# Kernel optimization log

Hardware: AMD Instinct MI355X
Metric: run time of the kernel (lower is better)

The kernel has to match this reference:

```python
import jax, jax.numpy as jnp
import numpy as np

B, C, H, W = 8, 64, 128, 128
NH, OPH = 4, 16
MX, MY = 32, 17  # n_modes=(32,32) -> modes_y = 32//2+1
NPAT_S, NPAT_F = 10000, 5000
ED_S, ED_F = 64, 32


def setup_inputs() -> dict:
    ks = jax.random.split(jax.random.key(0), 16)
    n = lambda k, s, sc=1.0: jax.random.normal(k, s, dtype=jnp.float32) * sc
    z = lambda s: jnp.zeros(s, jnp.float32)
    return dict(
        x=n(ks[0], (B, C, H, W)),
        se_emb=n(ks[1], (NPAT_S, ED_S)),
        se_w=n(ks[2], (ED_S, C), 0.1), se_b=z(C),
        mhf_wr=n(ks[3], (NH, C, OPH, MX, MY), 0.01),
        mhf_wi=n(ks[4], (NH, C, OPH, MX, MY), 0.01),
        mhf_bias=z(C),
        sp_emb=n(ks[5], (NPAT_F, ED_F)),
        sp_wr=n(ks[6], (ED_F, C * MX * MY), 0.05), sp_br=z(C * MX * MY),
        sp_wi=n(ks[7], (ED_F, C * MX * MY), 0.05), sp_bi=z(C * MX * MY),
        gate_w1=n(ks[8], (3 * C, 64), 0.05), gate_b1=z(64),
        gate_w2=n(ks[9], (64, 3), 0.05), gate_b2=z(3),
        skip_w=n(ks[10], (C, C), 0.05), skip_b=z(C),
        norm_g=jnp.ones(C), norm_b=z(C),
        mlp_w1=n(ks[11], (C, 2 * C), 0.05), mlp_b1=z(2 * C),
        mlp_w2=n(ks[12], (2 * C, C), 0.05), mlp_b2=z(C),
    )


def _gelu(v):
    return jax.nn.gelu(v, approximate=False)


def _block(x, se_emb, se_w, se_b, mhf_wr, mhf_wi, mhf_bias, sp_emb, sp_wr, sp_br,
           sp_wi, sp_bi, gate_w1, gate_b1, gate_w2, gate_b2, skip_w, skip_b,
           norm_g, norm_b, mlp_w1, mlp_b1, mlp_w2, mlp_b2):
    Bq, Cq, Hq, Wq = x.shape
    # --- SpatialEngram: quantization is elementwise, so sum over window entries
    # equals 3x3 box-sum of the quantized padded field (identical integers,
    # avoids materializing the (B,C,H,W,3,3) unfold tensor).
    xp = jnp.pad(x, ((0, 0), (0, 0), (1, 1), (1, 1)), mode='edge')
    q = (xp * 100.0).astype(jnp.int32)  # trunc toward zero, same as torch .long()
    hv = jnp.zeros((Bq, Cq, Hq, Wq), jnp.int32)
    for i in range(3):
        for j in range(3):
            hv = hv + q[:, :, i:i + Hq, j:j + Wq]
    idx = (jnp.abs(hv) % NPAT_S).astype(jnp.float32).mean(axis=1).astype(jnp.int32)  # (B,H,W)
    spatial = jnp.moveaxis(se_emb[idx] @ se_w + se_b, -1, 1)  # (B,C,H,W)
    # --- MHF multi-head spectral conv (all heads in one einsum; concat == reshape)
    xf = jnp.fft.rfft2(x, norm='ortho')          # (B,C,H,W//2+1) complex64
    lo = xf[:, :, :MX, :MY]
    wc = (mhf_wr + 1j * mhf_wi).astype(lo.dtype)
    of = jnp.einsum('biXY,hioXY->bhoXY', lo, wc).reshape(Bq, Cq, MX, MY)
    full = jnp.zeros((Bq, Cq, Hq, Wq // 2 + 1), lo.dtype).at[:, :, :MX, :MY].set(of)
    mhf = jnp.fft.irfft2(full, s=(Hq, Wq), norm='ortho') + mhf_bias[:, None, None]
    # --- SpectralEngram: per-sample hash of low-freq magnitude -> embedding -> freq proj
    mag = jnp.abs(lo).mean(axis=(1, 2, 3))                       # (B,)
    fidx = (mag * 1000.0).astype(jnp.int32) % NPAT_F
    fe = sp_emb[fidx]                                            # (B,ED_F)
    re = (fe @ sp_wr + sp_br).reshape(Bq, Cq, MX, MY)
    im = (fe @ sp_wi + sp_bi).reshape(Bq, Cq, MX, MY)
    full2 = jnp.zeros((Bq, Cq, Hq, Wq // 2 + 1), lo.dtype).at[:, :, :MX, :MY].set(re + 1j * im)
    spec = jnp.fft.irfft2(full2, s=(Hq, Wq), norm='ortho')
    # --- gated fusion
    gate_in = jnp.concatenate([spatial.mean((2, 3)), mhf.mean((2, 3)), spec.mean((2, 3))], axis=-1)
    gw = jax.nn.softmax(_gelu(gate_in @ gate_w1 + gate_b1) @ gate_w2 + gate_b2, axis=-1)
    a = gw[:, 0, None, None, None]
    bt = gw[:, 1, None, None, None]
    gm = gw[:, 2, None, None, None]
    fused = a * spatial + bt * mhf + gm * spec
    y = fused + jnp.einsum('bihw,io->bohw', x, skip_w) + skip_b[:, None, None]
    # --- GroupNorm(1,C) + 1x1-conv channel MLP (dropout=0)
    mu = y.mean((1, 2, 3), keepdims=True)
    var = y.var((1, 2, 3), keepdims=True)
    yn = (y - mu) * jax.lax.rsqrt(var + 1e-5) * norm_g[:, None, None] + norm_b[:, None, None]
    h = _gelu(jnp.einsum('bihw,io->bohw', yn, mlp_w1) + mlp_b1[:, None, None])
    h = jnp.einsum('bihw,io->bohw', h, mlp_w2) + mlp_b2[:, None, None]
    return y + h


def reference(x, se_emb, se_w, se_b, mhf_wr, mhf_wi, mhf_bias, sp_emb, sp_wr, sp_br,
              sp_wi, sp_bi, gate_w1, gate_b1, gate_w2, gate_b2, skip_w, skip_b,
              norm_g, norm_b, mlp_w1, mlp_b1, mlp_w2, mlp_b2):
    return _block(x, se_emb, se_w, se_b, mhf_wr, mhf_wi, mhf_bias, sp_emb, sp_wr, sp_br,
                  sp_wi, sp_bi, gate_w1, gate_b1, gate_w2, gate_b2, skip_w, skip_b,
                  norm_g, norm_b, mlp_w1, mlp_b1, mlp_w2, mlp_b2)
```

## Files before the change

### kernel.cpp

```cpp
#include <hip/hip_runtime.h>
#include <hip/hip_bf16.h>
#include <math.h>

#define B_ 8
#define C_ 64
#define H_ 128
#define W_ 128
#define NH_ 4
#define OPH_ 16
#define MX_ 32
#define MY_ 17
#define NPAT_F 5000
#define ED_F 32
#define XY_ (MX_*MY_)
#define HW_ (H_*W_)
#define NE_ (B_*C_*H_*W_)

#define OFF_LO     0u
#define OFF_T2     2228224u
#define OFF_FMHF   11141120u
#define OFF_FSPEC  13369344u
#define OFF_IDX    15597568u

typedef __hip_bfloat16 bf16;

template<typename T>
__device__ __forceinline__ float ldt(const void* p, int i){ return (float)(((const T*)p)[i]); }

__device__ __forceinline__ float gelu_f(float a){
  return 0.5f*a*(1.0f + erff(a*0.70710678118654752f));
}

__global__ void k_det(const void* ng, int* flag, double* dmag){
  if(threadIdx.x==0) *flag = (((const unsigned*)ng)[0] == 0x3F800000u) ? 1 : 0;
  if(threadIdx.x<B_) dmag[threadIdx.x] = 0.0;
}

template<typename T>
__device__ __forceinline__ void hash_body(const void* x, int* idx, int b, int h, int w){
  int hm = h>0 ? h-1 : 0, hp = h<127 ? h+1 : 127;
  int wm = w>0 ? w-1 : 0, wp = w<127 ? w+1 : 127;
  int s = 0;
  for(int c=0;c<C_;++c){
    const int base = ((b*C_+c)*H_)*W_;
    const int r0 = base + hm*W_, r1 = base + h*W_, r2 = base + hp*W_;
    int q = (int)(ldt<T>(x,r0+wm)*100.0f) + (int)(ldt<T>(x,r0+w)*100.0f) + (int)(ldt<T>(x,r0+wp)*100.0f)
          + (int)(ldt<T>(x,r1+wm)*100.0f) + (int)(ldt<T>(x,r1+w)*100.0f) + (int)(ldt<T>(x,r1+wp)*100.0f)
          + (int)(ldt<T>(x,r2+wm)*100.0f) + (int)(ldt<T>(x,r2+w)*100.0f) + (int)(ldt<T>(x,r2+wp)*100.0f);
    s += (q < 0 ? -q : q) % 10000;
  }
  idx[(b*H_+h)*W_+w] = s >> 6;
}
__global__ __launch_bounds__(128) void k_hash(const void* x, int* idx, const int* flg){
  int h = blockIdx.x, b = blockIdx.y, w = threadIdx.x;
  if(*flg) hash_body<float>(x, idx, b, h, w); else hash_body<bf16>(x, idx, b, h, w);
}

__global__ __launch_bounds__(256) void k_f1(const void* __restrict__ x, double* __restrict__ t1,
                                            const int* flg, int b0){
  __shared__ float xs[64*130];
  __shared__ double2 csd[128];
  int t = threadIdx.x;
  if(t<128){ double a = (double)t * (6.283185307179586476925286766559/128.0); csd[t] = make_double2(cos(a), sin(a)); }
  int hhalf = blockIdx.x, bcl = blockIdx.y;
  int h0 = hhalf << 6;
  long xbase = ((long)(b0*C_ + bcl)*H_ + h0)*W_;
  if(*flg){
    const float* xp = (const float*)x + xbase;
    for(int i=t;i<4096;i+=256){
      int r=i>>6, w2=(i&63)<<1;
      *(float2*)(xs + r*130 + w2) = *(const float2*)(xp + r*W_ + w2);
    }
  } else {
    const unsigned short* xp = (const unsigned short*)x + xbase;
    for(int i=t;i<4096;i+=256){
      int r=i>>6, w2=(i&63)<<1;
      unsigned raw = *(const unsigned*)(xp + r*W_ + w2);
      float2 v; v.x = __uint_as_float(raw<<16); v.y = __uint_as_float(raw & 0xffff0000u);
      *(float2*)(xs + r*130 + w2) = v;
    }
  }
  __syncthreads();
  for(int o=t;o<MY_*64;o+=256){
    int ky = o>>6, hr = o&63;
    const float* xr = xs + hr*130;
    double ar=0.0, ai=0.0;
    int m = 0;
    for(int w=0;w<W_;++w){
      double v = (double)xr[w];
      double2 cs2 = csd[m];
      ar = fma(v, cs2.x, ar);
      ai = fma(-v, cs2.y, ai);
      m = (m + ky) & 127;
    }
    int tt = (bcl*MY_ + ky)*H_ + (h0 + hr);
    *(double2*)(t1 + 2*tt) = make_double2(ar, ai);
  }
}

__global__ __launch_bounds__(576) void k_f2(const double* __restrict__ t1, float* __restrict__ lo, int b0){
  __shared__ double2 ts[MY_*129];
  __shared__ double2 csd[128];
  int t = threadIdx.x;
  if(t<128){ double a = (double)t * (6.283185307179586476925286766559/128.0); csd[t] = make_double2(cos(a), sin(a)); }
  int bcl = blockIdx.x;
  const double2* tg = (const double2*)t1 + (size_t)bcl*MY_*H_;
  for(int i=t;i<MY_*H_;i+=576){ int ky=i>>7, hh=i&127; ts[ky*129+hh] = tg[i]; }
  __syncthreads();
  if(t < 544){
    int ky = t % MY_, kx = t / MY_;
    const double2* tr = ts + ky*129;
    double ar=0.0, ai=0.0;
    int m = 0;
    for(int h=0;h<H_;++h){
      double2 v = tr[h];
      double2 cs2 = csd[m];
      double vr = v.x, vi = v.y;
      double cc = cs2.x, ss = cs2.y;
      ar += vr*cc + vi*ss;
      ai += vi*cc - vr*ss;
      m = (m + kx) & 127;
    }
    int g = (b0*C_ + bcl)*XY_ + kx*MY_ + ky;
    *(float2*)(lo + 2*g) = make_float2((float)(ar*(1.0/128.0)), (float)(ai*(1.0/128.0)));
  }
}

template<typename T>
__device__ __forceinline__ void spatial_load_w(const void* se_w, const void* se_b, float wsm[64][64], float* sb, int t){
  for(int i=t;i<4096;i+=256) wsm[i>>6][i&63] = ldt<T>(se_w, i);
  if(t<64) sb[t] = ldt<T>(se_b, t);
}
template<typename T>
__device__ __forceinline__ void spatial_load_emb(const void* se_emb, const int* ibs, float emb[32][65], int w0, int t){
  for(int i=t;i<2048;i+=256){ int wl_=i>>6, e=i&63; emb[wl_][e] = ldt<T>(se_emb, ibs[w0+wl_]*64 + e); }
}
__global__ __launch_bounds__(256) void k_spatial(const void* se_emb, const void* se_w, const void* se_b,
                                                 const int* __restrict__ idx, bf16* __restrict__ spatial,
                                                 const int* flg){
  __shared__ float wsm[64][64];
  __shared__ float emb[32][65];
  __shared__ float sb[64];
  __shared__ int ibs[128];
  int b = blockIdx.x >> 7, h = blockIdx.x & 127, t = threadIdx.x;
  int f = *flg;
  if(f) spatial_load_w<float>(se_w, se_b, wsm, sb, t); else spatial_load_w<bf16>(se_w, se_b, wsm, sb, t);
  if(t<128) ibs[t] = idx[(b*H_+h)*W_ + t];
  __syncthreads();
  for(int chunk=0; chunk<4; ++chunk){
    int w0 = chunk*32;
    if(f) spatial_load_emb<float>(se_emb, ibs, emb, w0, t); else spatial_load_emb<bf16>(se_emb, ibs, emb, w0, t);
    __syncthreads();
    for(int i=t;i<2048;i+=256){
      int cc=i>>5, wl_=i&31;
      float acc = sb[cc];
      #pragma unroll 8
      for(int e=0;e<64;++e) acc = fmaf(emb[wl_][e], wsm[e][cc], acc);
      spatial[((b*C_+cc)*H_+h)*W_ + w0+wl_] = __float2bfloat16(acc);
    }
    __syncthreads();
  }
}

__global__ __launch_bounds__(256) void k_mag(const float* __restrict__ lo, double* __restrict__ dmag){
  int b = blockIdx.y, t = threadIdx.x;
  const float* p = lo + b*C_*XY_*2;
  double s = 0.0;
  for(int i = blockIdx.x*256 + t; i < C_*XY_; i += 17*256){
    double re = p[2*i], im = p[2*i+1];
    s += sqrt(re*re + im*im);
  }
  __shared__ double sh[256];
  sh[t] = s; __syncthreads();
  for(int k=128;k>0;k>>=1){ if(t<k) sh[t]+=sh[t+k]; __syncthreads(); }
  if(t==0) atomicAdd(&dmag[b], sh[0]);
}

template<typename T>
__device__ __forceinline__ void specf_body(const void* sp_emb, const void* sp_wr, const void* sp_br,
                                           const void* sp_wi, const void* sp_bi, const double* dmag,
                                           float* fspec, float* fe, int b, int j, int t){
  double mag = dmag[b] / (double)(C_*XY_);
  int fv = ((int)(mag*1000.0)) % NPAT_F;
  fv = fv < 0 ? 0 : (fv >= NPAT_F ? NPAT_F-1 : fv);
  if(t < ED_F) fe[t] = ldt<T>(sp_emb, fv*ED_F + t);
  __syncthreads();
  float re = ldt<T>(sp_br, j), im = ldt<T>(sp_bi, j);
  #pragma unroll 8
  for(int e=0;e<ED_F;++e){
    float f = fe[e];
    re = fmaf(f, ldt<T>(sp_wr, e*(C_*XY_)+j), re);
    im = fmaf(f, ldt<T>(sp_wi, e*(C_*XY_)+j), im);
  }
  int o = b*C_*XY_ + j;
  fspec[2*o] = re; fspec[2*o+1] = im;
}
__global__ __launch_bounds__(256) void k_specf(const void* sp_emb, const void* sp_wr, const void* sp_br,
                                               const void* sp_wi, const void* sp_bi, const double* __restrict__ dmag,
                                               float* __restrict__ fspec, const int* flg){
  __shared__ float fe[ED_F];
  int b = blockIdx.y;
  int j = blockIdx.x*256 + threadIdx.x;
  if(*flg) specf_body<float>(sp_emb, sp_wr, sp_br, sp_wi, sp_bi, dmag, fspec, fe, b, j, threadIdx.x);
  else     specf_body<bf16 >(sp_emb, sp_wr, sp_br, sp_wi, sp_bi, dmag, fspec, fe, b, j, threadIdx.x);
}

template<typename T>
__device__ __forceinline__ void mhf_body(const float* lp, const void* wr, const void* wi,
                                         float* fmhf, int b, int co){
  int hh = co >> 4, o = co & 15;
  for(int xy = threadIdx.x; xy < XY_; xy += 256){
    float ar=0.f, ai=0.f;
    for(int i=0;i<C_;++i){
      float lr = lp[(i*XY_+xy)*2], li = lp[(i*XY_+xy)*2+1];
      int widx = ((hh*C_ + i)*OPH_ + o)*XY_ + xy;
      float wre = ldt<T>(wr, widx), wim = ldt<T>(wi, widx);
      ar += lr*wre - li*wim;
      ai += lr*wim + li*wre;
    }
    int oo = (b*C_ + co)*XY_ + xy;
    fmhf[2*oo] = ar; fmhf[2*oo+1] = ai;
  }
}
__global__ __launch_bounds__(256) void k_mhf(const float* __restrict__ lo, const void* wr, const void* wi,
                                             float* __restrict__ fmhf, const int* flg){
  int b = blockIdx.y, co = blockIdx.x;
  const float* lp = lo + b*C_*XY_*2;
  if(*flg) mhf_body<float>(lp, wr, wi, fmhf, b, co); else mhf_body<bf16>(lp, wr, wi, fmhf, b, co);
}

__global__ __launch_bounds__(256) void k_gmean(const bf16* __restrict__ spatial, float* __restrict__ smean){
  int cch = blockIdx.x, b = blockIdx.y, t = threadIdx.x;
  const unsigned short* p = (const unsigned short*)(spatial + (size_t)(b*C_+cch)*HW_);
  float s = 0.f;
  for(int i=t;i<HW_/8;i+=256){
    uint4 v = *(const uint4*)(p + (size_t)i*8);
    s += __uint_as_float(v.x<<16) + __uint_as_float(v.x&0xffff0000u)
       + __uint_as_float(v.y<<16) + __uint_as_float(v.y&0xffff0000u)
       + __uint_as_float(v.z<<16) + __uint_as_float(v.z&0xffff0000u)
       + __uint_as_float(v.w<<16) + __uint_as_float(v.w&0xffff0000u);
  }
  __shared__ float sh[256];
  sh[t]=s; __syncthreads();
  for(int k=128;k>0;k>>=1){ if(t<k) sh[t]+=sh[t+k]; __syncthreads(); }
  if(t==0) smean[b*C_+cch] = sh[0]*(1.0f/16384.0f);
}

template<typename T>
__device__ __forceinline__ void gate_body(const float* smean, const float* fmhf, const float* fspec,
                                          const void* mbias, const void* w1, const void* b1,
                                          const void* w2, const void* b2,
                                          float* gw, float* ssum, float* ssq,
                                          float* gin, float* hid, int b, int t){
  gin[t]      = smean[b*C_+t];
  gin[64+t]   = fmhf [(b*C_+t)*XY_*2] * (1.0f/128.0f) + ldt<T>(mbias, t);
  gin[128+t]  = fspec[(b*C_+t)*XY_*2] * (1.0f/128.0f);
  __syncthreads();
  float acc = ldt<T>(b1, t);
  for(int k=0;k<192;++k) acc = fmaf(gin[k], ldt<T>(w1, k*64+t), acc);
  hid[t] = gelu_f(acc);
  __syncthreads();
  if(t==0){
    float o[3];
    for(int j=0;j<3;++j){
      float a = ldt<T>(b2, j);
      for(int k=0;k<64;++k) a += hid[k]*ldt<T>(w2, k*3+j);
      o[j]=a;
    }
    float mx = fmaxf(o[0], fmaxf(o[1], o[2]));
    float e0=expf(o[0]-mx), e1=expf(o[1]-mx), e2=expf(o[2]-mx);
    float sum=e0+e1+e2;
    gw[b*3+0]=e0/sum; gw[b*3+1]=e1/sum; gw[b*3+2]=e2/sum;
    ssum[b]=0.f; ssq[b]=0.f;
  }
}
__global__ __launch_bounds__(64) void k_gate(const float* __restrict__ smean, const float* __restrict__ fmhf,
                                             const float* __restrict__ fspec, const void* mbias,
                                             const void* w1, const void* b1, const void* w2, const void* b2,
                                             float* __restrict__ gw, float* __restrict__ ssum,
                                             float* __restrict__ ssq, const int* flg){
  __shared__ float gin[192];
  __shared__ float hid[64];
  int b = blockIdx.x, t = threadIdx.x;
  if(*flg) gate_body<float>(smean, fmhf, fspec, mbias, w1, b1, w2, b2, gw, ssum, ssq, gin, hid, b, t);
  else     gate_body<bf16 >(smean, fmhf, fspec, mbias, w1, b1, w2, b2, gw, ssum, ssq, gin, hid, b, t);
}

__global__ __launch_bounds__(256) void k_comb(const float* __restrict__ fmhf, const float* __restrict__ fspec,
                                              const float* __restrict__ gw, float* __restrict__ t2){
  __shared__ float Gr[XY_], Gi[XY_], cs[128], sn[128];
  int c = blockIdx.x, b = blockIdx.y, t = threadIdx.x;
  if(t<128) __sincosf((float)t * 0.04908738521234052f, &sn[t], &cs[t]);
  float bt=gw[b*3+1], gm=gw[b*3+2];
  for(int i=t;i<XY_;i+=256){
    int o = ((b*C_+c)*XY_+i)*2;
    Gr[i] = bt*fmhf[o]   + gm*fspec[o];
    Gi[i] = bt*fmhf[o+1] + gm*fspec[o+1];
  }
  __syncthreads();
  for(int i=t;i<MY_*H_;i+=256){
    int hh = i & 127, ky = i >> 7;
    float ar=0.f, ai=0.f;
    for(int kx=0;kx<MX_;++kx){
      int m = (kx*hh)&127;
      float cc=cs[m], ss=sn[m];
      float fr=Gr[kx*MY_+ky], fi=Gi[kx*MY_+ky];
      ar += fr*cc - fi*ss;
      ai += fr*ss + fi*cc;
    }
    int e = (((b*C_+c)*MY_+ky)*H_ + hh)*2;
    t2[e]=ar; t2[e+1]=ai;
  }
}

template<typename T>
__device__ __forceinline__ void fuse_body(const void* x, const void* skw, const void* skb, const void* mbias,
                                          bf16* sp_y, const float* t2, const float* gw,
                                          float* ssum, float* ssq,
                                          float wl[64][64], float Ur[64][17], float Ui[64][17],
                                          float* cs, float* sn, float* sb, float* mb,
                                          float* s1, float* s2, int b, int h, int t){
  int w = t & 127, half = t >> 7;
  if(t<128) __sincosf((float)t * 0.04908738521234052f, &sn[t], &cs[t]);
  for(int i=t;i<4096;i+=256) wl[i>>6][i&63] = ldt<T>(skw, i);
  if(t<64){ sb[t]=ldt<T>(skb,t); mb[t]=ldt<T>(mbias,t); }
  for(int i=t;i<C_*MY_;i+=256){
    int cc=i/MY_, ky=i%MY_;
    int e = (((b*C_+cc)*MY_+ky)*H_ + h)*2;
    Ur[cc][ky]=t2[e]; Ui[cc][ky]=t2[e+1];
  }
  float ga=gw[b*3], gbv=gw[b*3+1];
  __syncthreads();
  int c0 = half*32;
  float acc[32];
  #pragma unroll
  for(int j=0;j<32;++j) acc[j]=sb[c0+j];
  int xb = (b*C_*H_ + h)*W_ + w;
  for(int k=0;k<64;++k){
    float xv = ldt<T>(x, xb + k*HW_);
    #pragma unroll
    for(int j=0;j<32;++j) acc[j] = fmaf(xv, wl[k][c0+j], acc[j]);
  }
  float ls=0.f, lq=0.f;
  for(int j=0;j<32;++j){
    int cc=c0+j;
    float vr = Ur[cc][0];
    #pragma unroll
    for(int ky=1;ky<MY_;++ky){
      int m=(ky*w)&127;
      vr += 2.0f*(Ur[cc][ky]*cs[m] - Ui[cc][ky]*sn[m]);
    }
    int gi = ((b*C_+cc)*H_+h)*W_+w;
    float v = ga*__bfloat162float(sp_y[gi]) + vr*(1.0f/128.0f) + gbv*mb[cc] + acc[j];
    sp_y[gi] = __float2bfloat16(v);
    ls += v; lq = fmaf(v, v, lq);
  }
  s1[t]=ls; s2[t]=lq; __syncthreads();
  for(int k=128;k>0;k>>=1){ if(t<k){ s1[t]+=s1[t+k]; s2[t]+=s2[t+k]; } __syncthreads(); }
  if(t==0){ atomicAdd(&ssum[b], s1[0]); atomicAdd(&ssq[b], s2[0]); }
}
__global__ __launch_bounds__(256) void k_fuse(const void* x, const void* skw, const void* skb, const void* mbias,
                                              bf16* __restrict__ sp_y, const float* __restrict__ t2,
                                              const float* __restrict__ gw,
                                              float* __restrict__ ssum, float* __restrict__ ssq, const int* flg){
  __shared__ float wl[64][64];
  __shared__ float Ur[64][17], Ui[64][17];
  __shared__ float cs[128], sn[128];
  __shared__ float sb[64], mb[64];
  __shared__ float s1[256], s2[256];
  int h = blockIdx.x, b = blockIdx.y, t = threadIdx.x;
  if(*flg) fuse_body<float>(x, skw, skb, mbias, sp_y, t2, gw, ssum, ssq, wl, Ur, Ui, cs, sn, sb, mb, s1, s2, b, h, t);
  else     fuse_body<bf16 >(x, skw, skb, mbias, sp_y, t2, gw, ssum, ssq, wl, Ur, Ui, cs, sn, sb, mb, s1, s2, b, h, t);
}

__global__ void k_stats(const float* __restrict__ ssum, const float* __restrict__ ssq,
                        float* __restrict__ mu, float* __restrict__ rs){
  int b = threadIdx.x;
  if(b < B_){
    float m = ssum[b] * (1.0f/1048576.0f);
    float v = ssq[b] * (1.0f/1048576.0f) - m*m;
    mu[b] = m;
    rs[b] = rsqrtf(v + 1e-5f);
  }
}

template<typename T>
__device__ __forceinline__ void mlp_body(const bf16* __restrict__ y, float mu, float rs,
                                         const void* ng, const void* nb, const void* w1, const void* b1,
                                         const void* w2, const void* b2, float* __restrict__ out,
                                         float* __restrict__ yn_s, float* __restrict__ w_s,
                                         float* __restrict__ h2_s,
                                         int b, int h, int w0, int t){
  const int tx = t & 15, ty = t >> 4;
  const int p0 = ty << 2;
  const int ybase = (b*C_*H_ + h)*W_ + w0;

  for(int i=t;i<8192;i+=256) w_s[i] = ldt<T>(w1, i);
  for(int it=0; it<4; ++it){
    int chunk = t + (it<<8);
    int c = chunk >> 4, p4 = (chunk & 15) << 2;
    const unsigned short* yp = (const unsigned short*)y + ybase + c*HW_ + p4;
    uint2 raw = *(const uint2*)yp;
    float g = ldt<T>(ng, c), nbv = ldt<T>(nb, c);
    float sc = rs*g;
    float4 o;
    o.x = (__uint_as_float(raw.x<<16)          - mu)*sc + nbv;
    o.y = (__uint_as_float(raw.x & 0xffff0000u)- mu)*sc + nbv;
    o.z = (__uint_as_float(raw.y<<16)          - mu)*sc + nbv;
    o.w = (__uint_as_float(raw.y & 0xffff0000u)- mu)*sc + nbv;
    *(float4*)(yn_s + c*68 + p4) = o;
  }
  float w2r[32];
  #pragma unroll
  for(int j=0;j<32;++j) w2r[j] = ldt<T>(w2, t + (j<<8));
  __syncthreads();

  const int kA = tx << 2, kB = 64 + (tx << 2);
  float a[8][4];
  #pragma unroll
  for(int j=0;j<4;++j){
    float bj = ldt<T>(b1, kA+j);
    a[j][0]=bj; a[j][1]=bj; a[j][2]=bj; a[j][3]=bj;
    float bj2 = ldt<T>(b1, kB+j);
    a[4+j][0]=bj2; a[4+j][1]=bj2; a[4+j][2]=bj2; a[4+j][3]=bj2;
  }
  #pragma unroll 8
  for(int i=0;i<64;++i){
    float4 yv = *(const float4*)(yn_s + i*68 + p0);
    float4 wa = *(const float4*)(w_s + (i<<7) + kA);
    float4 wb = *(const float4*)(w_s + (i<<7) + kB);
    float y4[4] = {yv.x, yv.y, yv.z, yv.w};
    float w8[8] = {wa.x, wa.y, wa.z, wa.w, wb.x, wb.y, wb.z, wb.w};
    #pragma unroll
    for(int j=0;j<8;++j){
      #pragma unroll
      for(int q=0;q<4;++q) a[j][q] = fmaf(y4[q], w8[j], a[j][q]);
    }
  }
  __syncthreads();

  #pragma unroll
  for(int j=0;j<32;++j) w_s[t + (j<<8)] = w2r[j];
  #pragma unroll
  for(int j=0;j<4;++j){
    float4 hA;
    hA.x = gelu_f(a[j][0]); hA.y = gelu_f(a[j][1]); hA.z = gelu_f(a[j][2]); hA.w = gelu_f(a[j][3]);
    *(float4*)(yn_s + (kA+j)*68 + p0) = hA;
    float4 hB;
    hB.x = gelu_f(a[4+j][0]); hB.y = gelu_f(a[4+j][1]); hB.z = gelu_f(a[4+j][2]); hB.w = gelu_f(a[4+j][3]);
    *(float4*)(h2_s + (kA+j)*68 + p0) = hB;
  }
  __syncthreads();

  const int c0 = tx << 2;
  float acc[4][4];
  #pragma unroll
  for(int j=0;j<4;++j){ acc[j][0]=0.f; acc[j][1]=0.f; acc[j][2]=0.f; acc[j][3]=0.f; }
  #pragma unroll 8
  for(int k=0;k<64;++k){
    float4 hv = *(const float4*)(yn_s + k*68 + p0);
    float4 wv = *(const float4*)(w_s + (k<<6) + c0);
    float hq[4] = {hv.x, hv.y, hv.z, hv.w};
    float w4[4] = {wv.x, wv.y, wv.z, wv.w};
    #pragma unroll
    for(int j=0;j<4;++j){
      #pragma unroll
      for(int q=0;q<4;++q) acc[j][q] = fmaf(hq[q], w4[j], acc[j][q]);
    }
  }
  #pragma unroll 8
  for(int k=0;k<64;++k){
    float4 hv = *(const float4*)(h2_s + k*68 + p0);
    float4 wv = *(const float4*)(w_s + ((64+k)<<6) + c0);
    float hq[4] = {hv.x, hv.y, hv.z, hv.w};
    float w4[4] = {wv.x, wv.y, wv.z, wv.w};
    #pragma unroll
    for(int j=0;j<4;++j){
      #pragma unroll
      for(int q=0;q<4;++q) acc[j][q] = fmaf(hq[q], w4[j], acc[j][q]);
    }
  }

  #pragma unroll
  for(int j=0;j<4;++j){
    int c = c0 + j;
    float b2v = ldt<T>(b2, c);
    const unsigned short* yp = (const unsigned short*)y + ybase + c*HW_ + p0;
    uint2 raw = *(const uint2*)yp;
    float4 o;
    o.x = __uint_as_float(raw.x<<16)           + acc[j][0] + b2v;
    o.y = __uint_as_float(raw.x & 0xffff0000u) + acc[j][1] + b2v;
    o.z = __uint_as_float(raw.y<<16)           + acc[j][2] + b2v;
    o.w = __uint_as_float(raw.y & 0xffff0000u) + acc[j][3] + b2v;
    *(float4*)(out + ybase + c*HW_ + p0) = o;
  }
}
__global__ __launch_bounds__(256) void k_mlp(const bf16* __restrict__ y, const float* __restrict__ mu_,
                                             const float* __restrict__ rs_, const void* ng, const void* nb,
                                             const void* w1, const void* b1, const void* w2, const void* b2,
                                             float* __restrict__ out, const int* flg){
  __shared__ float yn_s[64*68];
  __shared__ float w_s[8192];
  __shared__ float h2_s[64*68];
  int h = blockIdx.x >> 1, w0 = (blockIdx.x & 1) << 6, b = blockIdx.y;
  int t = threadIdx.x;
  float mu = mu_[b], rs = rs_[b];
  if(*flg) mlp_body<float>(y, mu, rs, ng, nb, w1, b1, w2, b2, out, yn_s, w_s, h2_s, b, h, w0, t);
  else     mlp_body<bf16 >(y, mu, rs, ng, nb, w1, b1, w2, b2, out, yn_s, w_s, h2_s, b, h, w0, t);
}

extern "C" void kernel_launch(void* const* d_in, const int* in_sizes, int n_in,
                              void* d_out, int out_size, void* d_ws, size_t ws_size,
                              hipStream_t stream) {
  (void)out_size; (void)ws_size;
  static const int dict_sizes[24] = {8388608,640000,4096,64,2228224,2228224,64,160000,
                                     1114112,34816,1114112,34816,12288,64,192,3,
                                     4096,64,64,64,8192,128,8192,64};
  static const int sorted_sizes[24] = {64,3,12288,192,64,2228224,2228224,128,64,8192,8192,
                                       64,64,64,640000,4096,64,4096,34816,34816,160000,
                                       1114112,1114112,8388608};
  static const int sorted_to_dict[24] = {13,15,12,14,6,5,4,21,23,20,22,19,18,3,1,2,17,16,11,9,7,10,8,0};

  const void* in[24];
  bool is_dict = (n_in == 24), is_sorted = (n_in == 24);
  if(n_in == 24){
    for(int i=0;i<24;++i){
      if(in_sizes[i] != dict_sizes[i])   is_dict   = false;
      if(in_sizes[i] != sorted_sizes[i]) is_sorted = false;
    }
  }
  if(is_sorted && !is_dict){
    for(int i=0;i<24;++i) in[sorted_to_dict[i]] = d_in[i];
  } else {
    for(int i=0;i<24 && i<n_in;++i) in[i] = d_in[i];
  }

  const void* x       = in[0];
  const void* se_emb  = in[1];
  const void* se_w    = in[2];
  const void* se_b    = in[3];
  const void* mhf_wr  = in[4];
  const void* mhf_wi  = in[5];
  const void* mhf_bias= in[6];
  const void* sp_emb  = in[7];
  const void* sp_wr   = in[8];
  const void* sp_br   = in[9];
  const void* sp_wi   = in[10];
  const void* sp_bi   = in[11];
  const void* gate_w1 = in[12];
  const void* gate_b1 = in[13];
  const void* gate_w2 = in[14];
  const void* gate_b2 = in[15];
  const void* skip_w  = in[16];
  const void* skip_b  = in[17];
  const void* norm_g  = in[18];
  const void* norm_b  = in[19];
  const void* mlp_w1  = in[20];
  const void* mlp_b1  = in[21];
  const void* mlp_w2  = in[22];
  const void* mlp_b2  = in[23];
  float* out = (float*)d_out;

  double* t1   = (double*)d_ws;
  bf16*   sp_y = (bf16*)d_ws;
  float*  scal = (float*)((char*)d_ws + (size_t)NE_*2);
  float* smean = scal;
  float* gw    = scal + 512;
  float* ssum  = scal + 536;
  float* ssq   = scal + 544;
  float* mu    = scal + 552;
  float* rs    = scal + 560;
  int*   flag  = (int*)(scal + 576);
  double* dmag = (double*)(scal + 584);

  char* ob = (char*)d_out;
  float* lo    = (float*)(ob + OFF_LO);
  float* t2    = (float*)(ob + OFF_T2);
  float* fmhf  = (float*)(ob + OFF_FMHF);
  float* fspec = (float*)(ob + OFF_FSPEC);
  int*   idx   = (int*)  (ob + OFF_IDX);

  hipLaunchKernelGGL(k_det,    dim3(1),           dim3(64),  0, stream, norm_g, flag, dmag);
  hipLaunchKernelGGL(k_hash,   dim3(H_, B_),      dim3(128), 0, stream, x, idx, flag);
  hipLaunchKernelGGL(k_f1,     dim3(2, 256),      dim3(256), 0, stream, x, t1, flag, 0);
  hipLaunchKernelGGL(k_f2,     dim3(256),         dim3(576), 0, stream, t1, lo, 0);
  hipLaunchKernelGGL(k_f1,     dim3(2, 256),      dim3(256), 0, stream, x, t1, flag, 4);
  hipLaunchKernelGGL(k_f2,     dim3(256),         dim3(576), 0, stream, t1, lo, 4);
  hipLaunchKernelGGL(k_spatial,dim3(B_*H_),       dim3(256), 0, stream, se_emb, se_w, se_b, idx, sp_y, flag);
  hipLaunchKernelGGL(k_mag,    dim3(17, B_),      dim3(256), 0, stream, lo, dmag);
  hipLaunchKernelGGL(k_specf,  dim3(C_*XY_/256, B_), dim3(256), 0, stream, sp_emb, sp_wr, sp_br, sp_wi, sp_bi, dmag, fspec, flag);
  hipLaunchKernelGGL(k_mhf,    dim3(C_, B_),      dim3(256), 0, stream, lo, mhf_wr, mhf_wi, fmhf, flag);
  hipLaunchKernelGGL(k_gmean,  dim3(C_, B_),      dim3(256), 0, stream, sp_y, smean);
  hipLaunchKernelGGL(k_gate,   dim3(B_),          dim3(64),  0, stream, smean, fmhf, fspec, mhf_bias, gate_w1, gate_b1, gate_w2, gate_b2, gw, ssum, ssq, flag);
  hipLaunchKernelGGL(k_comb,   dim3(C_, B_),      dim3(256), 0, stream, fmhf, fspec, gw, t2);
  hipLaunchKernelGGL(k_fuse,   dim3(H_, B_),      dim3(256), 0, stream, x, skip_w, skip_b, mhf_bias, sp_y, t2, gw, ssum, ssq, flag);
  hipLaunchKernelGGL(k_stats,  dim3(1),           dim3(64),  0, stream, ssum, ssq, mu, rs);
  hipLaunchKernelGGL(k_mlp,    dim3(H_*2, B_),    dim3(256), 0, stream, sp_y, mu, rs, norm_g, norm_b, mlp_w1, mlp_b1, mlp_w2, mlp_b2, out, flag);
}
```

Baseline: 520.6 us.

## Merge FFT batch halves, swizzle shared memory, vectorize loads, retile channel MLP

The first-stage DFT now runs over all batches in a single launch pair. Its intermediate buffer moves from the workspace into a larger region of the output buffer. k_f1 loads rows as float4 into an XOR-swizzled shared layout, which is meant to avoid bank conflicts and unroll the inner loop. Spectral-feature, MHF, combine and fuse kernels use paired float2/float4 loads and stores. The MLP kernel switches to 32-pixel tiles with twice as many blocks and swizzled weight layouts, which raises parallelism but loads weights into shared memory more often.

```diff
diff --git a/kernel.cpp b/kernel.cpp
--- a/kernel.cpp
+++ b/kernel.cpp
@@ -17,15 +17,23 @@
 #define NE_ (B_*C_*H_*W_)
 
 #define OFF_LO     0u
+#define OFF_T1     2228224u
 #define OFF_T2     2228224u
 #define OFF_FMHF   11141120u
 #define OFF_FSPEC  13369344u
-#define OFF_IDX    15597568u
+#define OFF_IDX    33030144u
 
 typedef __hip_bfloat16 bf16;
 
 template<typename T>
 __device__ __forceinline__ float ldt(const void* p, int i){ return (float)(((const T*)p)[i]); }
+
+template<typename T>
+__device__ __forceinline__ float2 ld2(const void* p, int i){
+  if(sizeof(T)==4) return *(const float2*)((const float*)p + i);
+  unsigned raw = *(const unsigned*)((const unsigned short*)p + i);
+  return make_float2(__uint_as_float(raw<<16), __uint_as_float(raw & 0xffff0000u));
+}
 
 __device__ __forceinline__ float gelu_f(float a){
   return 0.5f*a*(1.0f + erff(a*0.70710678118654752f));
@@ -57,48 +65,49 @@
 }
 
 __global__ __launch_bounds__(256) void k_f1(const void* __restrict__ x, double* __restrict__ t1,
-                                            const int* flg, int b0){
-  __shared__ float xs[64*130];
+                                            const int* flg){
+  __shared__ float4 xs4[2048];
   __shared__ double2 csd[128];
   int t = threadIdx.x;
   if(t<128){ double a = (double)t * (6.283185307179586476925286766559/128.0); csd[t] = make_double2(cos(a), sin(a)); }
-  int hhalf = blockIdx.x, bcl = blockIdx.y;
-  int h0 = hhalf << 6;
-  long xbase = ((long)(b0*C_ + bcl)*H_ + h0)*W_;
+  int h0 = blockIdx.x << 6, bcl = blockIdx.y;
+  long xbase = ((long)bcl*H_ + h0)*W_;
   if(*flg){
-    const float* xp = (const float*)x + xbase;
-    for(int i=t;i<4096;i+=256){
-      int r=i>>6, w2=(i&63)<<1;
-      *(float2*)(xs + r*130 + w2) = *(const float2*)(xp + r*W_ + w2);
+    const float4* xp = (const float4*)((const float*)x + xbase);
+    for(int i=t;i<2048;i+=256){
+      int r=i>>5, s=i&31;
+      xs4[(r<<5) + (s ^ (r&31))] = xp[i];
     }
   } else {
-    const unsigned short* xp = (const unsigned short*)x + xbase;
-    for(int i=t;i<4096;i+=256){
-      int r=i>>6, w2=(i&63)<<1;
-      unsigned raw = *(const unsigned*)(xp + r*W_ + w2);
-      float2 v; v.x = __uint_as_float(raw<<16); v.y = __uint_as_float(raw & 0xffff0000u);
-      *(float2*)(xs + r*130 + w2) = v;
+    const uint2* xp = (const uint2*)((const unsigned short*)x + xbase);
+    for(int i=t;i<2048;i+=256){
+      int r=i>>5, s=i&31;
+      uint2 raw = xp[i];
+      xs4[(r<<5) + (s ^ (r&31))] = make_float4(
+        __uint_as_float(raw.x<<16), __uint_as_float(raw.x & 0xffff0000u),
+        __uint_as_float(raw.y<<16), __uint_as_float(raw.y & 0xffff0000u));
     }
   }
   __syncthreads();
   for(int o=t;o<MY_*64;o+=256){
     int ky = o>>6, hr = o&63;
-    const float* xr = xs + hr*130;
+    const float4* xr = xs4 + (hr<<5);
+    const int sx = hr & 31;
     double ar=0.0, ai=0.0;
     int m = 0;
-    for(int w=0;w<W_;++w){
-      double v = (double)xr[w];
-      double2 cs2 = csd[m];
-      ar = fma(v, cs2.x, ar);
-      ai = fma(-v, cs2.y, ai);
-      m = (m + ky) & 127;
-    }
-    int tt = (bcl*MY_ + ky)*H_ + (h0 + hr);
+    for(int s=0;s<32;++s){
+      float4 v4 = xr[s ^ sx];
+      double2 c0 = csd[m]; ar = fma((double)v4.x, c0.x, ar); ai = fma(-(double)v4.x, c0.y, ai); m=(m+ky)&127;
+      double2 c1 = csd[m]; ar = fma((double)v4.y, c1.x, ar); ai = fma(-(double)v4.y, c1.y, ai); m=(m+ky)&127;
+      double2 c2 = csd[m]; ar = fma((double)v4.z, c2.x, ar); ai = fma(-(double)v4.z, c2.y, ai); m=(m+ky)&127;
+      double2 c3 = csd[m]; ar = fma((double)v4.w, c3.x, ar); ai = fma(-(double)v4.w, c3.y, ai); m=(m+ky)&127;
+    }
+    long tt = ((long)(bcl*MY_ + ky))*H_ + (h0 + hr);
     *(double2*)(t1 + 2*tt) = make_double2(ar, ai);
   }
 }
 
-__global__ __launch_bounds__(576) void k_f2(const double* __restrict__ t1, float* __restrict__ lo, int b0){
+__global__ __launch_bounds__(576) void k_f2(const double* __restrict__ t1, float* __restrict__ lo){
   __shared__ double2 ts[MY_*129];
   __shared__ double2 csd[128];
   int t = threadIdx.x;
@@ -121,7 +130,7 @@
       ai += vi*cc - vr*ss;
       m = (m + kx) & 127;
     }
-    int g = (b0*C_ + bcl)*XY_ + kx*MY_ + ky;
+    int g = bcl*XY_ + kx*MY_ + ky;
     *(float2*)(lo + 2*g) = make_float2((float)(ar*(1.0/128.0)), (float)(ai*(1.0/128.0)));
   }
 }
@@ -179,30 +188,33 @@
 template<typename T>
 __device__ __forceinline__ void specf_body(const void* sp_emb, const void* sp_wr, const void* sp_br,
                                            const void* sp_wi, const void* sp_bi, const double* dmag,
-                                           float* fspec, float* fe, int b, int j, int t){
+                                           float* fspec, float* fe, int b, int j0, int t){
   double mag = dmag[b] / (double)(C_*XY_);
   int fv = ((int)(mag*1000.0)) % NPAT_F;
   fv = fv < 0 ? 0 : (fv >= NPAT_F ? NPAT_F-1 : fv);
   if(t < ED_F) fe[t] = ldt<T>(sp_emb, fv*ED_F + t);
   __syncthreads();
-  float re = ldt<T>(sp_br, j), im = ldt<T>(sp_bi, j);
+  float2 rr = ld2<T>(sp_br, j0), ii = ld2<T>(sp_bi, j0);
+  float re0=rr.x, re1=rr.y, im0=ii.x, im1=ii.y;
   #pragma unroll 8
   for(int e=0;e<ED_F;++e){
     float f = fe[e];
-    re = fmaf(f, ldt<T>(sp_wr, e*(C_*XY_)+j), re);
-    im = fmaf(f, ldt<T>(sp_wi, e*(C_*XY_)+j), im);
-  }
-  int o = b*C_*XY_ + j;
-  fspec[2*o] = re; fspec[2*o+1] = im;
+    float2 wr = ld2<T>(sp_wr, e*(C_*XY_)+j0);
+    float2 wi = ld2<T>(sp_wi, e*(C_*XY_)+j0);
+    re0 = fmaf(f, wr.x, re0); im0 = fmaf(f, wi.x, im0);
+    re1 = fmaf(f, wr.y, re1); im1 = fmaf(f, wi.y, im1);
+  }
+  int o = b*C_*XY_ + j0;
+  *(float4*)(fspec + 2*o) = make_float4(re0, im0, re1, im1);
 }
 __global__ __launch_bounds__(256) void k_specf(const void* sp_emb, const void* sp_wr, const void* sp_br,
                                                const void* sp_wi, const void* sp_bi, const double* __restrict__ dmag,
                                                float* __restrict__ fspec, const int* flg){
   __shared__ float fe[ED_F];
   int b = blockIdx.y;
-  int j = blockIdx.x*256 + threadIdx.x;
-  if(*flg) specf_body<float>(sp_emb, sp_wr, sp_br, sp_wi, sp_bi, dmag, fspec, fe, b, j, threadIdx.x);
-  else     specf_body<bf16 >(sp_emb, sp_wr, sp_br, sp_wi, sp_bi, dmag, fspec, fe, b, j, threadIdx.x);
+  int j0 = (blockIdx.x*256 + threadIdx.x)*2;
+  if(*flg) specf_body<float>(sp_emb, sp_wr, sp_br, sp_wi, sp_bi, dmag, fspec, fe, b, j0, threadIdx.x);
+  else     specf_body<bf16 >(sp_emb, sp_wr, sp_br, sp_wi, sp_bi, dmag, fspec, fe, b, j0, threadIdx.x);
 }
 
 template<typename T>
@@ -212,14 +224,15 @@
   for(int xy = threadIdx.x; xy < XY_; xy += 256){
     float ar=0.f, ai=0.f;
     for(int i=0;i<C_;++i){
-      float lr = lp[(i*XY_+xy)*2], li = lp[(i*XY_+xy)*2+1];
+      float2 l2 = *(const float2*)(lp + (i*XY_+xy)*2);
+      float lr = l2.x, li = l2.y;
       int widx = ((hh*C_ + i)*OPH_ + o)*XY_ + xy;
       float wre = ldt<T>(wr, widx), wim = ldt<T>(wi, widx);
       ar += lr*wre - li*wim;
       ai += lr*wim + li*wre;
     }
     int oo = (b*C_ + co)*XY_ + xy;
-    fmhf[2*oo] = ar; fmhf[2*oo+1] = ai;
+    *(float2*)(fmhf + 2*oo) = make_float2(ar, ai);
   }
 }
 __global__ __launch_bounds__(256) void k_mhf(const float* __restrict__ lo, const void* wr, const void* wi,
@@ -294,8 +307,10 @@
   float bt=gw[b*3+1], gm=gw[b*3+2];
   for(int i=t;i<XY_;i+=256){
     int o = ((b*C_+c)*XY_+i)*2;
-    Gr[i] = bt*fmhf[o]   + gm*fspec[o];
-    Gi[i] = bt*fmhf[o+1] + gm*fspec[o+1];
+    float2 fm = *(const float2*)(fmhf + o);
+    float2 fs = *(const float2*)(fspec + o);
+    Gr[i] = bt*fm.x + gm*fs.x;
+    Gi[i] = bt*fm.y + gm*fs.y;
   }
   __syncthreads();
   for(int i=t;i<MY_*H_;i+=256){
@@ -309,7 +324,7 @@
       ai += fr*ss + fi*cc;
     }
     int e = (((b*C_+c)*MY_+ky)*H_ + hh)*2;
-    t2[e]=ar; t2[e+1]=ai;
+    *(float2*)(t2 + e) = make_float2(ar, ai);
   }
 }
 
@@ -327,7 +342,8 @@
   for(int i=t;i<C_*MY_;i+=256){
     int cc=i/MY_, ky=i%MY_;
     int e = (((b*C_+cc)*MY_+ky)*H_ + h)*2;
-    Ur[cc][ky]=t2[e]; Ui[cc][ky]=t2[e+1];
+    float2 v = *(const float2*)(t2 + e);
+    Ur[cc][ky]=v.x; Ui[cc][ky]=v.y;
   }
   float ga=gw[b*3], gbv=gw[b*3+1];
   __syncthreads();
@@ -391,14 +407,17 @@
                                          float* __restrict__ yn_s, float* __restrict__ w_s,
                                          float* __restrict__ h2_s,
                                          int b, int h, int w0, int t){
-  const int tx = t & 15, ty = t >> 4;
+  const int tx = t & 31, ty = t >> 5;
   const int p0 = ty << 2;
   const int ybase = (b*C_*H_ + h)*W_ + w0;
 
-  for(int i=t;i<8192;i+=256) w_s[i] = ldt<T>(w1, i);
-  for(int it=0; it<4; ++it){
-    int chunk = t + (it<<8);
-    int c = chunk >> 4, p4 = (chunk & 15) << 2;
+  for(int L=t; L<8192; L+=256){
+    int i = L>>7, j = L&127;
+    w_s[(i<<7) + (((j>>2) ^ (i&31))<<2) + (j&3)] = ldt<T>(w1, L);
+  }
+  for(int it=0; it<2; ++it){
+    int idx = t + (it<<8);
+    int c = idx>>3, p4 = (idx&7)<<2;
     const unsigned short* yp = (const unsigned short*)y + ybase + c*HW_ + p4;
     uint2 raw = *(const uint2*)yp;
     float g = ldt<T>(ng, c), nbv = ldt<T>(nb, c);
@@ -408,81 +427,79 @@
     o.y = (__uint_as_float(raw.x & 0xffff0000u)- mu)*sc + nbv;
     o.z = (__uint_as_float(raw.y<<16)          - mu)*sc + nbv;
     o.w = (__uint_as_float(raw.y & 0xffff0000u)- mu)*sc + nbv;
-    *(float4*)(yn_s + c*68 + p4) = o;
+    *(float4*)(yn_s + c*36 + p4) = o;
   }
   float w2r[32];
   #pragma unroll
-  for(int j=0;j<32;++j) w2r[j] = ldt<T>(w2, t + (j<<8));
-  __syncthreads();
-
-  const int kA = tx << 2, kB = 64 + (tx << 2);
-  float a[8][4];
+  for(int jj=0;jj<32;++jj) w2r[jj] = ldt<T>(w2, t + (jj<<8));
+  __syncthreads();
+
+  const int kA = tx << 2;
+  float a[4][4];
   #pragma unroll
   for(int j=0;j<4;++j){
     float bj = ldt<T>(b1, kA+j);
     a[j][0]=bj; a[j][1]=bj; a[j][2]=bj; a[j][3]=bj;
-    float bj2 = ldt<T>(b1, kB+j);
-    a[4+j][0]=bj2; a[4+j][1]=bj2; a[4+j][2]=bj2; a[4+j][3]=bj2;
-  }
-  #pragma unroll 8
+  }
+  #pragma unroll 4
   for(int i=0;i<64;++i){
-    float4 yv = *(const float4*)(yn_s + i*68 + p0);
-    float4 wa = *(const float4*)(w_s + (i<<7) + kA);
-    float4 wb = *(const float4*)(w_s + (i<<7) + kB);
+    float4 yv = *(const float4*)(yn_s + i*36 + p0);
+    float4 wv = *(const float4*)(w_s + (i<<7) + ((tx ^ (i&31))<<2));
     float y4[4] = {yv.x, yv.y, yv.z, yv.w};
-    float w8[8] = {wa.x, wa.y, wa.z, wa.w, wb.x, wb.y, wb.z, wb.w};
-    #pragma unroll
-    for(int j=0;j<8;++j){
-      #pragma unroll
-      for(int q=0;q<4;++q) a[j][q] = fmaf(y4[q], w8[j], a[j][q]);
-    }
-  }
-  __syncthreads();
-
-  #pragma unroll
-  for(int j=0;j<32;++j) w_s[t + (j<<8)] = w2r[j];
-  #pragma unroll
-  for(int j=0;j<4;++j){
-    float4 hA;
-    hA.x = gelu_f(a[j][0]); hA.y = gelu_f(a[j][1]); hA.z = gelu_f(a[j][2]); hA.w = gelu_f(a[j][3]);
-    *(float4*)(yn_s + (kA+j)*68 + p0) = hA;
-    float4 hB;
-    hB.x = gelu_f(a[4+j][0]); hB.y = gelu_f(a[4+j][1]); hB.z = gelu_f(a[4+j][2]); hB.w = gelu_f(a[4+j][3]);
-    *(float4*)(h2_s + (kA+j)*68 + p0) = hB;
-  }
-  __syncthreads();
-
-  const int c0 = tx << 2;
-  float acc[4][4];
-  #pragma unroll
-  for(int j=0;j<4;++j){ acc[j][0]=0.f; acc[j][1]=0.f; acc[j][2]=0.f; acc[j][3]=0.f; }
-  #pragma unroll 8
-  for(int k=0;k<64;++k){
-    float4 hv = *(const float4*)(yn_s + k*68 + p0);
-    float4 wv = *(const float4*)(w_s + (k<<6) + c0);
-    float hq[4] = {hv.x, hv.y, hv.z, hv.w};
     float w4[4] = {wv.x, wv.y, wv.z, wv.w};
     #pragma unroll
     for(int j=0;j<4;++j){
       #pragma unroll
-      for(int q=0;q<4;++q) acc[j][q] = fmaf(hq[q], w4[j], acc[j][q]);
-    }
-  }
-  #pragma unroll 8
+      for(int q=0;q<4;++q) a[j][q] = fmaf(y4[q], w4[j], a[j][q]);
+    }
+  }
+  __syncthreads();
+
+  #pragma unroll
+  for(int jj=0;jj<32;++jj){
+    int L = t + (jj<<8);
+    int k = L>>6, c = L&63;
+    w_s[(k<<6) + (((c>>1) ^ (k&31))<<1) + (c&1)] = w2r[jj];
+  }
+  {
+    float* hb = (tx < 16) ? yn_s : h2_s;
+    int rbase = (tx & 15) << 2;
+    #pragma unroll
+    for(int j=0;j<4;++j){
+      float4 hv;
+      hv.x = gelu_f(a[j][0]); hv.y = gelu_f(a[j][1]); hv.z = gelu_f(a[j][2]); hv.w = gelu_f(a[j][3]);
+      *(float4*)(hb + (rbase+j)*36 + p0) = hv;
+    }
+  }
+  __syncthreads();
+
+  const int c0 = tx << 1;
+  float acc[2][4];
+  #pragma unroll
+  for(int j=0;j<2;++j){ acc[j][0]=0.f; acc[j][1]=0.f; acc[j][2]=0.f; acc[j][3]=0.f; }
+  #pragma unroll 4
   for(int k=0;k<64;++k){
-    float4 hv = *(const float4*)(h2_s + k*68 + p0);
-    float4 wv = *(const float4*)(w_s + ((64+k)<<6) + c0);
+    float4 hv = *(const float4*)(yn_s + k*36 + p0);
+    float2 wv = *(const float2*)(w_s + (k<<6) + ((tx ^ (k&31))<<1));
     float hq[4] = {hv.x, hv.y, hv.z, hv.w};
-    float w4[4] = {wv.x, wv.y, wv.z, wv.w};
-    #pragma unroll
-    for(int j=0;j<4;++j){
-      #pragma unroll
-      for(int q=0;q<4;++q) acc[j][q] = fmaf(hq[q], w4[j], acc[j][q]);
-    }
+    #pragma unroll
+    for(int q=0;q<4;++q) acc[0][q] = fmaf(hq[q], wv.x, acc[0][q]);
+    #pragma unroll
+    for(int q=0;q<4;++q) acc[1][q] = fmaf(hq[q], wv.y, acc[1][q]);
+  }
+  #pragma unroll 4
+  for(int k=0;k<64;++k){
+    float4 hv = *(const float4*)(h2_s + k*36 + p0);
+    float2 wv = *(const float2*)(w_s + ((64+k)<<6) + ((tx ^ (k&31))<<1));
+    float hq[4] = {hv.x, hv.y, hv.z, hv.w};
+    #pragma unroll
+    for(int q=0;q<4;++q) acc[0][q] = fmaf(hq[q], wv.x, acc[0][q]);
+    #pragma unroll
+    for(int q=0;q<4;++q) acc[1][q] = fmaf(hq[q], wv.y, acc[1][q]);
   }
 
   #pragma unroll
-  for(int j=0;j<4;++j){
+  for(int j=0;j<2;++j){
     int c = c0 + j;
     float b2v = ldt<T>(b2, c);
     const unsigned short* yp = (const unsigned short*)y + ybase + c*HW_ + p0;
@@ -499,10 +516,10 @@
                                              const float* __restrict__ rs_, const void* ng, const void* nb,
                                              const void* w1, const void* b1, const void* w2, const void* b2,
                                              float* __restrict__ out, const int* flg){
-  __shared__ float yn_s[64*68];
+  __shared__ float yn_s[64*36];
   __shared__ float w_s[8192];
-  __shared__ float h2_s[64*68];
-  int h = blockIdx.x >> 1, w0 = (blockIdx.x & 1) << 6, b = blockIdx.y;
+  __shared__ float h2_s[64*36];
+  int h = blockIdx.x >> 2, w0 = (blockIdx.x & 3) << 5, b = blockIdx.y;
   int t = threadIdx.x;
   float mu = mu_[b], rs = rs_[b];
   if(*flg) mlp_body<float>(y, mu, rs, ng, nb, w1, b1, w2, b2, out, yn_s, w_s, h2_s, b, h, w0, t);
@@ -561,7 +578,6 @@
   const void* mlp_b2  = in[23];
   float* out = (float*)d_out;
 
-  double* t1   = (double*)d_ws;
   bf16*   sp_y = (bf16*)d_ws;
   float*  scal = (float*)((char*)d_ws + (size_t)NE_*2);
   float* smean = scal;
@@ -574,26 +590,25 @@
   double* dmag = (double*)(scal + 584);
 
   char* ob = (char*)d_out;
-  float* lo    = (float*)(ob + OFF_LO);
-  float* t2    = (float*)(ob + OFF_T2);
-  float* fmhf  = (float*)(ob + OFF_FMHF);
-  float* fspec = (float*)(ob + OFF_FSPEC);
-  int*   idx   = (int*)  (ob + OFF_IDX);
+  float*  lo    = (float*) (ob + OFF_LO);
+  double* t1    = (double*)(ob + OFF_T1);
+  float*  t2    = (float*) (ob + OFF_T2);
+  float*  fmhf  = (float*) (ob + OFF_FMHF);
+  float*  fspec = (float*) (ob + OFF_FSPEC);
+  int*    idx   = (int*)   (ob + OFF_IDX);
 
   hipLaunchKernelGGL(k_det,    dim3(1),           dim3(64),  0, stream, norm_g, flag, dmag);
   hipLaunchKernelGGL(k_hash,   dim3(H_, B_),      dim3(128), 0, stream, x, idx, flag);
-  hipLaunchKernelGGL(k_f1,     dim3(2, 256),      dim3(256), 0, stream, x, t1, flag, 0);
-  hipLaunchKernelGGL(k_f2,     dim3(256),         dim3(576), 0, stream, t1, lo, 0);
-  hipLaunchKernelGGL(k_f1,     dim3(2, 256),      dim3(256), 0, stream, x, t1, flag, 4);
-  hipLaunchKernelGGL(k_f2,     dim3(256),         dim3(576), 0, stream, t1, lo, 4);
+  hipLaunchKernelGGL(k_f1,     dim3(2, 512),      dim3(256), 0, stream, x, t1, flag);
+  hipLaunchKernelGGL(k_f2,     dim3(512),         dim3(576), 0, stream, t1, lo);
   hipLaunchKernelGGL(k_spatial,dim3(B_*H_),       dim3(256), 0, stream, se_emb, se_w, se_b, idx, sp_y, flag);
   hipLaunchKernelGGL(k_mag,    dim3(17, B_),      dim3(256), 0, stream, lo, dmag);
-  hipLaunchKernelGGL(k_specf,  dim3(C_*XY_/256, B_), dim3(256), 0, stream, sp_emb, sp_wr, sp_br, sp_wi, sp_bi, dmag, fspec, flag);
+  hipLaunchKernelGGL(k_specf,  dim3(C_*XY_/512, B_), dim3(256), 0, stream, sp_emb, sp_wr, sp_br, sp_wi, sp_bi, dmag, fspec, flag);
   hipLaunchKernelGGL(k_mhf,    dim3(C_, B_),      dim3(256), 0, stream, lo, mhf_wr, mhf_wi, fmhf, flag);
   hipLaunchKernelGGL(k_gmean,  dim3(C_, B_),      dim3(256), 0, stream, sp_y, smean);
   hipLaunchKernelGGL(k_gate,   dim3(B_),          dim3(64),  0, stream, smean, fmhf, fspec, mhf_bias, gate_w1, gate_b1, gate_w2, gate_b2, gw, ssum, ssq, flag);
   hipLaunchKernelGGL(k_comb,   dim3(C_, B_),      dim3(256), 0, stream, fmhf, fspec, gw, t2);
   hipLaunchKernelGGL(k_fuse,   dim3(H_, B_),      dim3(256), 0, stream, x, skip_w, skip_b, mhf_bias, sp_y, t2, gw, ssum, ssq, flag);
   hipLaunchKernelGGL(k_stats,  dim3(1),           dim3(64),  0, stream, ssum, ssq, mu, rs);
-  hipLaunchKernelGGL(k_mlp,    dim3(H_*2, B_),    dim3(256), 0, stream, sp_y, mu, rs, norm_g, norm_b, mlp_w1, mlp_b1, mlp_w2, mlp_b2, out, flag);
-}
+  hipLaunchKernelGGL(k_mlp,    dim3(H_*4, B_),    dim3(256), 0, stream, sp_y, mu, rs, norm_g, norm_b, mlp_w1, mlp_b1, mlp_w2, mlp_b2, out, flag);
+}
```

New measurement: 507.5 us. -2.5%, faster.
